# Kernel tuning notes

Hardware: AMD Instinct MI355X
Metric: run time of the kernel (lower is better)

## Reference

```python
import jax, jax.numpy as jnp
import numpy as np

B, S, DIM = 16, 8192, 128
H, KV, D = 4, 2, 64  # heads, kv_heads, dim_head


def setup_inputs() -> dict:
    key = jax.random.key(0)
    ks = jax.random.split(key, 8)
    scale = 0.05
    return {
        "x": jax.random.normal(ks[0], (B, S, DIM), dtype=jnp.float32),
        "Wq": jax.random.normal(ks[1], (H, D, DIM), dtype=jnp.float32) * scale,
        "bq": jax.random.normal(ks[2], (H, D), dtype=jnp.float32) * scale,
        "Wk": jax.random.normal(ks[3], (KV, D, DIM), dtype=jnp.float32) * scale,
        "bk": jax.random.normal(ks[4], (KV, D), dtype=jnp.float32) * scale,
        "Wv": jax.random.normal(ks[5], (KV, D, DIM), dtype=jnp.float32) * scale,
        "bv": jax.random.normal(ks[6], (KV, D), dtype=jnp.float32) * scale,
        "Wo": jax.random.normal(ks[7], (DIM, DIM), dtype=jnp.float32) * scale,
    }


def reference(x, Wq, bq, Wk, bk, Wv, bv, Wo):
    b, s, _ = x.shape
    # MultiHeadLinear: per-head Linear stacked on last axis -> [B,S,D,H]
    q_st = jnp.einsum("bsc,hdc->bsdh", x, Wq) + bq.T  # [B,S,D,H]
    k_st = jnp.einsum("bsc,hdc->bsdh", x, Wk) + bk.T  # [B,S,D,KV]
    v_st = jnp.einsum("bsc,hdc->bsdh", x, Wv) + bv.T  # [B,S,D,KV]
    # .view(B,-1,heads,dim_head): raw reshape of (D,H) block into (H,D)
    q = q_st.reshape(b, s, H, D)
    k = k_st.reshape(b, s, KV, D)
    v = v_st.reshape(b, s, KV, D)
    # k scaled by q mean over heads (no softmax anywhere)
    k = k * jnp.mean(q, axis=2, keepdims=True)  # [B,S,KV,D]
    attn = jnp.einsum("bshd,bskd->bshk", q, k) / jnp.sqrt(jnp.asarray(D, q.dtype))
    out = jnp.einsum("bshk,bskd->bshd", attn, v)  # [B,S,H,D]
    # reshape(B,-1,dim): [B,S,H*D=256] -> [B,2S,128]
    out = out.reshape(b, -1, DIM)
    return out @ Wo.T
```

## Files before the change

### kernel.cpp

```cpp
#include <hip/hip_runtime.h>
#include <stdint.h>


using short8 = __attribute__((ext_vector_type(8))) short;
using f32x4  = __attribute__((ext_vector_type(4))) float;

constexpr int XSTR = 136;
constexpr int PSTR = 12;
constexpr int T_TILES = 8;

__device__ __forceinline__ unsigned short f2bf(float f) {
    unsigned int u = __float_as_uint(f);
    u += 0x7FFFu + ((u >> 16) & 1u);
    return (unsigned short)(u >> 16);
}

__global__ void prep_weights(const float* __restrict__ Wq, const float* __restrict__ bq,
                             const float* __restrict__ Wk, const float* __restrict__ bk,
                             const float* __restrict__ Wv, const float* __restrict__ bv,
                             const float* __restrict__ Wo,
                             unsigned short* __restrict__ Wp, float* __restrict__ bias)
{
    const int ch = blockIdx.x;
    const int c  = threadIdx.x;
    float w, b;
    if (ch < 256) {
        const int hh = ch & 3, dd = ch >> 2;
        w = Wq[(hh * 64 + dd) * 128 + c];
        b = bq[hh * 64 + dd];
    } else if (ch < 384) {
        const int i = ch - 256;
        const int kvh = i & 1, dd = i >> 1;
        w = Wk[(kvh * 64 + dd) * 128 + c];
        b = bk[kvh * 64 + dd];
    } else {
        const int i  = ch - 384;
        const int jg = i >> 6, kp = (i >> 4) & 3, jm = i & 15;
        const int j  = jg * 16 + jm, kv = kp >> 1, p = kp & 1;
        float acc = 0.f, bacc = 0.f;
        #pragma unroll 8
        for (int d = 0; d < 64; ++d) {
            const int idx = kv * 64 + d;
            const int kvh = idx & 1, dd = idx >> 1;
            const float wo = Wo[j * 128 + p * 64 + d];
            acc  += wo * Wv[(kvh * 64 + dd) * 128 + c];
            bacc += wo * bv[kvh * 64 + dd];
        }
        w = acc; b = bacc;
    }
    Wp[ch * 128 + c] = f2bf(w);
    if (c == 0) bias[ch] = b;
}

__device__ __forceinline__ void stage8_load(const float* __restrict__ x, int tb, int row0,
                                            int l, float4* xv)
{
    const int row = row0 + (l >> 3);
    const float* src = x + (size_t)(tb + row) * 128 + (l & 7) * 4;
    #pragma unroll
    for (int j = 0; j < 4; ++j) xv[j] = *(const float4*)(src + 32 * j);
}
__device__ __forceinline__ void stage8_write(unsigned short* __restrict__ xb, int row0,
                                             int l, const float4* xv)
{
    const int row = row0 + (l >> 3);
    #pragma unroll
    for (int j = 0; j < 4; ++j) {
        ushort4 s;
        s.x = f2bf(xv[j].x); s.y = f2bf(xv[j].y); s.z = f2bf(xv[j].z); s.w = f2bf(xv[j].w);
        *(ushort4*)&xb[row * XSTR + (l & 7) * 4 + 32 * j] = s;
    }
}

__global__ __launch_bounds__(512, 2)
void fused_attn_kernel(const float* __restrict__ x,
                       const unsigned short* __restrict__ Wp,
                       const float* __restrict__ bias,
                       float* __restrict__ out)
{
    __shared__ __align__(16) unsigned short xlds[3][64 * XSTR];
    __shared__ __align__(16) float partial[2][4][64][PSTR];
    __shared__ __align__(16) float coeffw[4][64][8];
    __shared__ __align__(16) float obufs[4][1024];

    const int tid = threadIdx.x;
    const int l   = tid & 63;
    const int wv  = tid >> 6;
    const int lr  = l & 15, lg = l >> 4;
    const int tok0 = blockIdx.x * (T_TILES * 64);

    if (wv < 4) {
        const int dc = wv;
        int chb[6];
        #pragma unroll
        for (int n = 0; n < 4; ++n) chb[n] = n * 64 + dc * 16;
        chb[4] = 256 + dc * 16;
        chb[5] = 320 + dc * 16;

        short8 areg[24];
        #pragma unroll
        for (int n = 0; n < 6; ++n)
            #pragma unroll
            for (int ks = 0; ks < 4; ++ks)
                areg[n * 4 + ks] = *(const short8*)(Wp + (size_t)(chb[n] + lr) * 128 + ks * 32 + lg * 8);
        f32x4 biasv[6];
        #pragma unroll
        for (int n = 0; n < 6; ++n)
            biasv[n] = *(const f32x4*)(bias + chb[n] + lg * 4);

        auto phase1 = [&](const unsigned short* __restrict__ xb, int pb) {
            #pragma unroll
            for (int th = 0; th < 2; ++th) {
                f32x4 acc[2][6];
                #pragma unroll
                for (int ti = 0; ti < 2; ++ti)
                    #pragma unroll
                    for (int n = 0; n < 6; ++n)
                        acc[ti][n] = (f32x4){0.f, 0.f, 0.f, 0.f};
                #pragma unroll
                for (int ks = 0; ks < 4; ++ks) {
                    #pragma unroll
                    for (int ti = 0; ti < 2; ++ti) {
                        const int tf = th * 2 + ti;
                        short8 bfr = *(const short8*)&xb[(tf * 16 + lr) * XSTR + ks * 32 + lg * 8];
                        #pragma unroll
                        for (int n = 0; n < 6; ++n)
                            acc[ti][n] = __builtin_amdgcn_mfma_f32_16x16x32_bf16(
                                areg[n * 4 + ks], bfr, acc[ti][n], 0, 0, 0);
                    }
                }
                #pragma unroll
                for (int ti = 0; ti < 2; ++ti) {
                    const int tf = th * 2 + ti;
                    float pa[8];
                    #pragma unroll
                    for (int c = 0; c < 8; ++c) pa[c] = 0.f;
                    #pragma unroll
                    for (int r = 0; r < 4; ++r) {
                        const float q0 = acc[ti][0][r] + biasv[0][r];
                        const float q1 = acc[ti][1][r] + biasv[1][r];
                        const float q2 = acc[ti][2][r] + biasv[2][r];
                        const float q3 = acc[ti][3][r] + biasv[3][r];
                        const float k0v = acc[ti][4][r] + biasv[4][r];
                        const float k1v = acc[ti][5][r] + biasv[5][r];
                        const float qm  = 0.25f * (q0 + q1 + q2 + q3);
                        const float kt0 = k0v * qm, kt1 = k1v * qm;
                        pa[0] += q0 * kt0; pa[1] += q1 * kt0;
                        pa[2] += q0 * kt1; pa[3] += q1 * kt1;
                        pa[4] += q2 * kt0; pa[5] += q3 * kt0;
                        pa[6] += q2 * kt1; pa[7] += q3 * kt1;
                    }
                    #pragma unroll
                    for (int c = 0; c < 8; ++c) pa[c] += __shfl_xor(pa[c], 16);
                    #pragma unroll
                    for (int c = 0; c < 8; ++c) pa[c] += __shfl_xor(pa[c], 32);
                    if (lg == 0) {
                        f32x4 p0 = {pa[0], pa[1], pa[2], pa[3]};
                        f32x4 p1 = {pa[4], pa[5], pa[6], pa[7]};
                        float* dst = &partial[pb][dc][tf * 16 + lr][0];
                        *(f32x4*)(dst)     = p0;
                        *(f32x4*)(dst + 4) = p1;
                    }
                }
            }
        };

        {
            float4 xv[4];
            stage8_load(x, tok0, wv * 8, l, xv);
            stage8_write(xlds[0], wv * 8, l, xv);
        }
        __syncthreads();
        phase1(xlds[0], 0);
        __syncthreads();

        for (int t = 0; t < T_TILES; ++t) {
            float4 xv[4];
            const bool do_stage = (t < T_TILES - 2);
            if (do_stage) stage8_load(x, tok0 + (t + 2) * 64, wv * 8, l, xv);
            if (t < T_TILES - 1) phase1(xlds[(t + 1) % 3], (t + 1) & 1);
            if (do_stage) stage8_write(xlds[(t + 2) % 3], wv * 8, l, xv);
            __syncthreads();
        }
    } else {
        const int jgp = wv - 4;

        short8 breg[32];
        #pragma unroll
        for (int j2 = 0; j2 < 2; ++j2)
            #pragma unroll
            for (int kp = 0; kp < 4; ++kp)
                #pragma unroll
                for (int ks = 0; ks < 4; ++ks)
                    breg[(j2 * 4 + kp) * 4 + ks] = *(const short8*)
                        (Wp + (size_t)(384 + (jgp * 2 + j2) * 64 + kp * 16 + lr) * 128 + ks * 32 + lg * 8);
        float bvv[2][4];
        #pragma unroll
        for (int j2 = 0; j2 < 2; ++j2)
            #pragma unroll
            for (int kp = 0; kp < 4; ++kp)
                bvv[j2][kp] = bias[384 + (jgp * 2 + j2) * 64 + kp * 16 + lr];

        auto phase2 = [&](const unsigned short* __restrict__ xb, int t) {
            const int g0    = tok0 + t * 64;
            const int bb    = g0 >> 13;
            const int srow0 = bb * 16384 + 2 * (g0 & 8191);
            #pragma unroll
            for (int mf = 0; mf < 4; ++mf) {
                f32x4 a2[2][4];
                #pragma unroll
                for (int j2 = 0; j2 < 2; ++j2)
                    #pragma unroll
                    for (int kp = 0; kp < 4; ++kp)
                        a2[j2][kp] = (f32x4){0.f, 0.f, 0.f, 0.f};
                #pragma unroll
                for (int ks = 0; ks < 4; ++ks) {
                    short8 af = *(const short8*)&xb[(mf * 16 + lr) * XSTR + ks * 32 + lg * 8];
                    #pragma unroll
                    for (int j2 = 0; j2 < 2; ++j2)
                        #pragma unroll
                        for (int kp = 0; kp < 4; ++kp)
                            a2[j2][kp] = __builtin_amdgcn_mfma_f32_16x16x32_bf16(
                                af, breg[(j2 * 4 + kp) * 4 + ks], a2[j2][kp], 0, 0, 0);
                }
                const int sw = (lg & 1) << 4;
                #pragma unroll
                for (int j2 = 0; j2 < 2; ++j2) {
                    #pragma unroll
                    for (int r = 0; r < 4; ++r) {
                        const int tokL = lg * 4 + r;
                        const int tok  = mf * 16 + tokL;
                        f32x4 cl = *(const f32x4*)&coeffw[jgp][tok][0];
                        f32x4 ch = *(const f32x4*)&coeffw[jgp][tok][4];
                        const float a0 = a2[j2][0][r] + bvv[j2][0];
                        const float a1 = a2[j2][1][r] + bvv[j2][1];
                        const float a2v = a2[j2][2][r] + bvv[j2][2];
                        const float a3 = a2[j2][3][r] + bvv[j2][3];
                        const float o0 = cl[0] * a0 + cl[1] * a1 + cl[2] * a2v + cl[3] * a3;
                        const float o1 = ch[0] * a0 + ch[1] * a1 + ch[2] * a2v + ch[3] * a3;
                        const int base = tokL * 64 + j2 * 16 + lr;
                        obufs[jgp][(base     ) ^ sw] = o0;
                        obufs[jgp][(base + 32) ^ sw] = o1;
                    }
                }
                #pragma unroll
                for (int i = 0; i < 4; ++i) {
                    const int w    = i * 256 + l * 4;
                    const int phys = w ^ (((w >> 8) & 1) << 4);
                    f32x4 vv = *(const f32x4*)&obufs[jgp][phys];
                    const int tokL = i * 4 + (l >> 4);
                    const int row  = srow0 + 32 * mf + 2 * tokL + ((l >> 3) & 1);
                    *(f32x4*)(out + (size_t)row * 128 + jgp * 32 + (l & 7) * 4) = vv;
                }
            }
        };

        {
            float4 xv[4];
            stage8_load(x, tok0, 32 + jgp * 8, l, xv);
            stage8_write(xlds[0], 32 + jgp * 8, l, xv);
        }
        __syncthreads();
        {
            float4 xv[4];
            stage8_load(x, tok0 + 64, jgp * 16, l, xv);
            stage8_write(xlds[1], jgp * 16, l, xv);
            stage8_load(x, tok0 + 64, jgp * 16 + 8, l, xv);
            stage8_write(xlds[1], jgp * 16 + 8, l, xv);
        }
        __syncthreads();

        for (int t = 0; t < T_TILES; ++t) {
            float4 xv[4];
            const bool do_stage = (t < T_TILES - 2);
            if (do_stage) stage8_load(x, tok0 + (t + 2) * 64, 32 + jgp * 8, l, xv);
            {
                const int pb = t & 1;
                float s[8];
                #pragma unroll
                for (int c = 0; c < 8; ++c) s[c] = 0.f;
                #pragma unroll
                for (int dcc = 0; dcc < 4; ++dcc) {
                    const float* pr = &partial[pb][dcc][l][0];
                    #pragma unroll
                    for (int c = 0; c < 8; ++c) s[c] += pr[c];
                }
                f32x4 c0 = {s[0] * 0.125f, s[1] * 0.125f, s[2] * 0.125f, s[3] * 0.125f};
                f32x4 c1 = {s[4] * 0.125f, s[5] * 0.125f, s[6] * 0.125f, s[7] * 0.125f};
                *(f32x4*)&coeffw[jgp][l][0] = c0;
                *(f32x4*)&coeffw[jgp][l][4] = c1;
            }
            phase2(xlds[t % 3], t);
            if (do_stage) stage8_write(xlds[(t + 2) % 3], 32 + jgp * 8, l, xv);
            __syncthreads();
        }
    }
}

extern "C" void kernel_launch(void* const* d_in, const int* in_sizes, int n_in,
                              void* d_out, int out_size, void* d_ws, size_t ws_size,
                              hipStream_t stream)
{
    (void)in_sizes; (void)n_in; (void)out_size; (void)ws_size;
    const float* x  = (const float*)d_in[0];
    const float* Wq = (const float*)d_in[1];
    const float* bq = (const float*)d_in[2];
    const float* Wk = (const float*)d_in[3];
    const float* bk = (const float*)d_in[4];
    const float* Wv = (const float*)d_in[5];
    const float* bv = (const float*)d_in[6];
    const float* Wo = (const float*)d_in[7];

    unsigned short* Wp   = (unsigned short*)d_ws;
    float*          bias = (float*)((char*)d_ws + 896 * 128 * 2);

    prep_weights<<<896, 128, 0, stream>>>(Wq, bq, Wk, bk, Wv, bv, Wo, Wp, bias);
    fused_attn_kernel<<<256, 512, 0, stream>>>(x, Wp, bias, (float*)d_out);
}
```

Before: 61.42 us.

## Permute fused Wo columns to store output directly and use non-draining barriers

Reorders the fused Wv·Wo weight rows in the prep kernel so each lane's MFMA results map to adjacent output columns. The output can then be written straight from registers as float2 stores, with no LDS staging buffer and shuffle readback. It also replaces __syncthreads with an inline-asm barrier that waits only on LDS counters, so outstanding global loads and stores are not drained at each barrier. The risks are narrower global stores, and depending on the asm barrier being correct for the LDS hazards.

```diff
diff --git a/kernel.cpp b/kernel.cpp
--- a/kernel.cpp
+++ b/kernel.cpp
@@ -13,6 +13,10 @@
     unsigned int u = __float_as_uint(f);
     u += 0x7FFFu + ((u >> 16) & 1u);
     return (unsigned short)(u >> 16);
+}
+
+__device__ __forceinline__ void barrier_nodrain() {
+    asm volatile("s_waitcnt lgkmcnt(0)\n\ts_barrier" ::: "memory");
 }
 
 __global__ void prep_weights(const float* __restrict__ Wq, const float* __restrict__ bq,
@@ -36,7 +40,8 @@
     } else {
         const int i  = ch - 384;
         const int jg = i >> 6, kp = (i >> 4) & 3, jm = i & 15;
-        const int j  = jg * 16 + jm, kv = kp >> 1, p = kp & 1;
+        const int j  = (jg >> 1) * 32 + jm * 2 + (jg & 1);
+        const int kv = kp >> 1, p = kp & 1;
         float acc = 0.f, bacc = 0.f;
         #pragma unroll 8
         for (int d = 0; d < 64; ++d) {
@@ -81,7 +86,6 @@
     __shared__ __align__(16) unsigned short xlds[3][64 * XSTR];
     __shared__ __align__(16) float partial[2][4][64][PSTR];
     __shared__ __align__(16) float coeffw[4][64][8];
-    __shared__ __align__(16) float obufs[4][1024];
 
     const int tid = threadIdx.x;
     const int l   = tid & 63;
@@ -170,9 +174,9 @@
             stage8_load(x, tok0, wv * 8, l, xv);
             stage8_write(xlds[0], wv * 8, l, xv);
         }
-        __syncthreads();
+        barrier_nodrain();
         phase1(xlds[0], 0);
-        __syncthreads();
+        barrier_nodrain();
 
         for (int t = 0; t < T_TILES; ++t) {
             float4 xv[4];
@@ -180,7 +184,7 @@
             if (do_stage) stage8_load(x, tok0 + (t + 2) * 64, wv * 8, l, xv);
             if (t < T_TILES - 1) phase1(xlds[(t + 1) % 3], (t + 1) & 1);
             if (do_stage) stage8_write(xlds[(t + 2) % 3], wv * 8, l, xv);
-            __syncthreads();
+            barrier_nodrain();
         }
     } else {
         const int jgp = wv - 4;
@@ -223,34 +227,33 @@
                             a2[j2][kp] = __builtin_amdgcn_mfma_f32_16x16x32_bf16(
                                 af, breg[(j2 * 4 + kp) * 4 + ks], a2[j2][kp], 0, 0, 0);
                 }
-                const int sw = (lg & 1) << 4;
-                #pragma unroll
-                for (int j2 = 0; j2 < 2; ++j2) {
-                    #pragma unroll
-                    for (int r = 0; r < 4; ++r) {
-                        const int tokL = lg * 4 + r;
-                        const int tok  = mf * 16 + tokL;
-                        f32x4 cl = *(const f32x4*)&coeffw[jgp][tok][0];
-                        f32x4 ch = *(const f32x4*)&coeffw[jgp][tok][4];
-                        const float a0 = a2[j2][0][r] + bvv[j2][0];
-                        const float a1 = a2[j2][1][r] + bvv[j2][1];
-                        const float a2v = a2[j2][2][r] + bvv[j2][2];
-                        const float a3 = a2[j2][3][r] + bvv[j2][3];
-                        const float o0 = cl[0] * a0 + cl[1] * a1 + cl[2] * a2v + cl[3] * a3;
-                        const float o1 = ch[0] * a0 + ch[1] * a1 + ch[2] * a2v + ch[3] * a3;
-                        const int base = tokL * 64 + j2 * 16 + lr;
-                        obufs[jgp][(base     ) ^ sw] = o0;
-                        obufs[jgp][(base + 32) ^ sw] = o1;
-                    }
-                }
-                #pragma unroll
-                for (int i = 0; i < 4; ++i) {
-                    const int w    = i * 256 + l * 4;
-                    const int phys = w ^ (((w >> 8) & 1) << 4);
-                    f32x4 vv = *(const f32x4*)&obufs[jgp][phys];
-                    const int tokL = i * 4 + (l >> 4);
-                    const int row  = srow0 + 32 * mf + 2 * tokL + ((l >> 3) & 1);
-                    *(f32x4*)(out + (size_t)row * 128 + jgp * 32 + (l & 7) * 4) = vv;
+                #pragma unroll
+                for (int r = 0; r < 4; ++r) {
+                    const int tokL = lg * 4 + r;
+                    const int tok  = mf * 16 + tokL;
+                    f32x4 cl = *(const f32x4*)&coeffw[jgp][tok][0];
+                    f32x4 ch = *(const f32x4*)&coeffw[jgp][tok][4];
+                    float2 s0, s1;
+                    {
+                        const float a0 = a2[0][0][r] + bvv[0][0];
+                        const float a1 = a2[0][1][r] + bvv[0][1];
+                        const float av = a2[0][2][r] + bvv[0][2];
+                        const float a3 = a2[0][3][r] + bvv[0][3];
+                        s0.x = cl[0] * a0 + cl[1] * a1 + cl[2] * av + cl[3] * a3;
+                        s1.x = ch[0] * a0 + ch[1] * a1 + ch[2] * av + ch[3] * a3;
+                    }
+                    {
+                        const float a0 = a2[1][0][r] + bvv[1][0];
+                        const float a1 = a2[1][1][r] + bvv[1][1];
+                        const float av = a2[1][2][r] + bvv[1][2];
+                        const float a3 = a2[1][3][r] + bvv[1][3];
+                        s0.y = cl[0] * a0 + cl[1] * a1 + cl[2] * av + cl[3] * a3;
+                        s1.y = ch[0] * a0 + ch[1] * a1 + ch[2] * av + ch[3] * a3;
+                    }
+                    const int row = srow0 + 32 * mf + 2 * tokL;
+                    float* dst = out + (size_t)row * 128 + jgp * 32 + lr * 2;
+                    *(float2*)(dst)       = s0;
+                    *(float2*)(dst + 128) = s1;
                 }
             }
         };
@@ -260,7 +263,7 @@
             stage8_load(x, tok0, 32 + jgp * 8, l, xv);
             stage8_write(xlds[0], 32 + jgp * 8, l, xv);
         }
-        __syncthreads();
+        barrier_nodrain();
         {
             float4 xv[4];
             stage8_load(x, tok0 + 64, jgp * 16, l, xv);
@@ -268,7 +271,7 @@
             stage8_load(x, tok0 + 64, jgp * 16 + 8, l, xv);
             stage8_write(xlds[1], jgp * 16 + 8, l, xv);
         }
-        __syncthreads();
+        barrier_nodrain();
 
         for (int t = 0; t < T_TILES; ++t) {
             float4 xv[4];
@@ -292,7 +295,7 @@
             }
             phase2(xlds[t % 3], t);
             if (do_stage) stage8_write(xlds[(t + 2) % 3], 32 + jgp * 8, l, xv);
-            __syncthreads();
+            barrier_nodrain();
         }
     }
 }
```

Result: faster. 56.35 us (-8.3%).
